# Kernel tuning notes

Hardware: AMD Instinct MI355X
Metric: run time of the kernel (lower is better)

## Reference

```python
import jax, jax.numpy as jnp
import numpy as np

BUCKETS = 256
B, CIN, H, W = 16, 64, 128, 128
COUT, K = 64, 3


def setup_inputs() -> dict:
    key = jax.random.key(0)
    k1, k2, k3, k4, k5 = jax.random.split(key, 5)
    x = jax.random.normal(k1, (B, CIN, H, W), dtype=jnp.float32)
    x_hash = jax.random.normal(k2, (B, CIN, H, W), dtype=jnp.float32)
    conv_weight = jax.random.normal(k3, (COUT, CIN, K, K), dtype=jnp.float32)
    hash_value = jnp.sort(jax.random.normal(k4, (BUCKETS,), dtype=jnp.float32))
    bias = jax.random.normal(k5, (COUT,), dtype=jnp.float32) * 0.1
    return {"x": x, "x_hash": x_hash, "conv_weight": conv_weight,
            "hash_value": hash_value, "bias": bias}


def _conv(x, w, b):
    # stride 1, padding 1 -> same spatial size (matches nn.Conv2d(padding=1))
    y = jax.lax.conv_general_dilated(
        x, w, window_strides=(1, 1), padding=[(1, 1), (1, 1)],
        dimension_numbers=("NCHW", "OIHW", "NCHW"))
    return y + b[None, :, None, None]


def _hash_weights(conv_weight, hash_value):
    # Uniform bucketization of weights into BUCKETS bins over [min, max],
    # then gather of the learned per-bucket hash value.
    w_min = jnp.min(conv_weight)
    w_max = jnp.max(conv_weight)
    width = (w_max - w_min) / BUCKETS
    idx = jnp.floor((conv_weight - w_min) / width).astype(jnp.int32)
    # w == max floors to BUCKETS; torch code assigns it the last bucket.
    idx = jnp.clip(idx, 0, BUCKETS - 1)
    return jnp.take(hash_value, idx)


def reference(x, x_hash, conv_weight, hash_value, bias):
    hash_weight = _hash_weights(conv_weight, hash_value)
    out = _conv(x, conv_weight, bias)
    hash_out = _conv(x, hash_weight, bias)
    out_hash = _conv(x_hash, hash_weight, bias)
    return (out, hash_out, out_hash)
```

## Files before the change

kernel.cpp:

```cpp
#include <hip/hip_runtime.h>
#include <stdint.h>

typedef short short8_t __attribute__((ext_vector_type(8)));
typedef float f32x4    __attribute__((ext_vector_type(4)));

__device__ __forceinline__ unsigned short f2bf(float f) {
  unsigned int u = __float_as_uint(f);
  u += 0x7FFFu + ((u >> 16) & 1u);
  return (unsigned short)(u >> 16);
}

__device__ __forceinline__ void glld16(const void* src, char* lds) {
  __builtin_amdgcn_global_load_lds(
      (const __attribute__((address_space(1))) void*)src,
      (__attribute__((address_space(3))) void*)lds, 16, 0, 0);
}

__device__ __forceinline__ short8_t lds_rd(const char* smem, int a) {
  int aa = a ^ (((a >> 7) & 7) << 4);
  return *(const short8_t*)(smem + aa);
}

__global__ __launch_bounds__(256) void minmax_kernel(const float* __restrict__ w,
                                                     float* __restrict__ mm) {
  int tid = threadIdx.x;
  float mn = 1e30f, mx = -1e30f;
  const float4* w4 = (const float4*)w;
  for (int i = tid; i < 9216; i += 256) {
    float4 v = w4[i];
    mn = fminf(mn, fminf(fminf(v.x, v.y), fminf(v.z, v.w)));
    mx = fmaxf(mx, fmaxf(fmaxf(v.x, v.y), fmaxf(v.z, v.w)));
  }
  for (int off = 32; off; off >>= 1) {
    mn = fminf(mn, __shfl_down(mn, off));
    mx = fmaxf(mx, __shfl_down(mx, off));
  }
  __shared__ float smn[4], smx[4];
  if ((tid & 63) == 0) { smn[tid >> 6] = mn; smx[tid >> 6] = mx; }
  __syncthreads();
  if (tid == 0) {
    mn = fminf(fminf(smn[0], smn[1]), fminf(smn[2], smn[3]));
    mx = fmaxf(fmaxf(smx[0], smx[1]), fmaxf(smx[2], smx[3]));
    mm[0] = mn; mm[1] = mx;
  }
}

__global__ __launch_bounds__(256) void hashprep_kernel(const float* __restrict__ w,
                                                       const float* __restrict__ hv,
                                                       const float* __restrict__ mm,
                                                       unsigned short* __restrict__ w0,
                                                       unsigned short* __restrict__ w1) {
  int t = blockIdx.x * 256 + threadIdx.x;
  if (t >= 36864) return;
  float mn = mm[0], mx = mm[1];
  float width = (mx - mn) / 256.0f;
  float wv = w[t];
  int idx = (int)floorf((wv - mn) / width);
  idx = min(max(idx, 0), 255);
  float hw = hv[idx];
  int co  = t / 576;
  int rem = t - co * 576;
  int ci  = rem / 9;
  int tap = rem - ci * 9;
  int dst = (tap * 64 + co) * 64 + ci;
  w0[dst] = f2bf(wv);
  w1[dst] = f2bf(hw);
}

__global__ __launch_bounds__(256) void xprep_kernel(const float* __restrict__ x,
                                                    unsigned short* __restrict__ xbf) {
  int t = blockIdx.x * 256 + threadIdx.x;
  int c8 = t & 7;
  int w  = (t >> 3) % 130;
  int bh = (t >> 3) / 130;
  short8_t v;
  #pragma unroll
  for (int j = 0; j < 8; ++j) v[j] = 0;
  if (w != 0 && w != 129) {
    const float* p = x + (((size_t)(bh >> 7) * 64 + c8 * 8) * 128 + (bh & 127)) * 128 + (w - 1);
    #pragma unroll
    for (int j = 0; j < 8; ++j) v[j] = (short)f2bf(p[(size_t)j * 16384]);
  }
  *(short8_t*)(xbf + (size_t)t * 8) = v;
}

#define XROW 16640
#define WSB  99840

template<int NSETS>
__global__ __launch_bounds__(512, 2) void conv_kernel(
    const unsigned short* __restrict__ xbf,
    const char* __restrict__ zeropage,
    const unsigned short* __restrict__ wg0,
    const unsigned short* __restrict__ wg1,
    const float* __restrict__ bias,
    float* __restrict__ out0,
    float* __restrict__ out1) {

  extern __shared__ char smem[];
  const int BUFSTRIDE = NSETS * 8192;

  int tid = threadIdx.x, lane = tid & 63, wv = tid >> 6;
  int m = lane & 15, g = (lane >> 4) & 3;
  int rr = wv >> 1, wseg = (wv & 1) << 6;

  int bx = blockIdx.x;
  int b = bx >> 5, h0 = (bx & 31) << 2;

  const char* xb = (const char*)xbf + (size_t)b * (130 * 128 * 128);
  for (int batch = wv; batch < 98; batch += 8) {
    int q = batch * 64 + lane;
    if (q < 6240) {
      int r    = q / 1040;
      int o_in = (q - r * 1040) << 4;
      int swz  = o_in ^ (((q >> 3) & 7) << 4);
      int hin  = h0 + r - 1;
      const char* src = ((unsigned)hin < 128u) ? (xb + (size_t)hin * XROW + swz)
                                               : (zeropage + swz);
      glld16(src, smem + batch * 1024);
    }
  }

  auto stage_w = [&](int t, int buf) {
    for (int batch = wv; batch < NSETS * 8; batch += 8) {
      int q    = batch * 64 + lane;
      int s    = q >> 9;
      int o_in = (q & 511) << 4;
      int key  = (4 + (q >> 3)) & 7;
      int swz  = o_in ^ (key << 4);
      const char* src = (const char*)(s ? wg1 : wg0) + t * 8192 + swz;
      glld16(src, smem + WSB + buf * BUFSTRIDE + batch * 1024);
    }
  };

  f32x4 acc[NSETS][4][4];
  #pragma unroll
  for (int s = 0; s < NSETS; ++s)
    #pragma unroll
    for (int i = 0; i < 4; ++i)
      #pragma unroll
      for (int j = 0; j < 4; ++j) acc[s][i][j] = (f32x4){0.f, 0.f, 0.f, 0.f};

  int arow[4], bcol[4];
  #pragma unroll
  for (int i = 0; i < 4; ++i) {
    arow[i] = ((i * 16 + m) << 7) + (g << 4);
    bcol[i] = ((wseg + i * 16 + m) << 7) + (g << 4);
  }

  stage_w(0, 0);
  __syncthreads();

  #pragma unroll
  for (int t = 0; t < 9; ++t) {
    if (t < 8) stage_w(t + 1, (t + 1) & 1);
    int kh = t / 3, kw = t - kh * 3;
    int xtap  = (rr + kh) * XROW + (kw << 7);
    int wbase = WSB + (t & 1) * BUFSTRIDE;
    #pragma unroll
    for (int ks = 0; ks < 2; ++ks) {
      int ko = ks << 6;
      short8_t bf[4];
      #pragma unroll
      for (int nf = 0; nf < 4; ++nf) bf[nf] = lds_rd(smem, xtap + bcol[nf] + ko);
      #pragma unroll
      for (int mt = 0; mt < 4; ++mt) {
        short8_t a0 = lds_rd(smem, wbase + arow[mt] + ko);
        #pragma unroll
        for (int nf = 0; nf < 4; ++nf)
          acc[0][mt][nf] = __builtin_amdgcn_mfma_f32_16x16x32_bf16(a0, bf[nf], acc[0][mt][nf], 0, 0, 0);
        if (NSETS == 2) {
          short8_t a1 = lds_rd(smem, wbase + 8192 + arow[mt] + ko);
          #pragma unroll
          for (int nf = 0; nf < 4; ++nf)
            acc[1][mt][nf] = __builtin_amdgcn_mfma_f32_16x16x32_bf16(a1, bf[nf], acc[1][mt][nf], 0, 0, 0);
        }
      }
    }
    __syncthreads();
  }

  size_t ob = (size_t)b * 64 * 16384 + (size_t)(h0 + rr) * 128 + wseg;
  #pragma unroll
  for (int s = 0; s < NSETS; ++s) {
    float* op = s ? out1 : out0;
    #pragma unroll
    for (int mt = 0; mt < 4; ++mt)
      #pragma unroll
      for (int r4 = 0; r4 < 4; ++r4) {
        int co = mt * 16 + g * 4 + r4;
        float bv = bias[co];
        #pragma unroll
        for (int nf = 0; nf < 4; ++nf)
          op[ob + (size_t)co * 16384 + nf * 16 + m] = acc[s][mt][nf][r4] + bv;
      }
  }
}

extern "C" void kernel_launch(void* const* d_in, const int* in_sizes, int n_in,
                              void* d_out, int out_size, void* d_ws, size_t ws_size,
                              hipStream_t stream) {
  const float* x    = (const float*)d_in[0];
  const float* xh   = (const float*)d_in[1];
  const float* cw   = (const float*)d_in[2];
  const float* hv   = (const float*)d_in[3];
  const float* bias = (const float*)d_in[4];

  float* out      = (float*)d_out;
  float* hash_out = out + 16777216;
  float* out_hash = out + 33554432;

  char* ws = (char*)d_ws;
  float* mm            = (float*)ws;
  char* zeropage       = ws + 128;
  unsigned short* w0   = (unsigned short*)(ws + 32768);
  unsigned short* w1   = (unsigned short*)(ws + 32768 + 73728);
  unsigned short* xbf  = (unsigned short*)(ws + 180224);

  hipMemsetAsync(zeropage, 0, 16640, stream);
  minmax_kernel<<<1, 256, 0, stream>>>(cw, mm);
  hashprep_kernel<<<144, 256, 0, stream>>>(cw, hv, mm, w0, w1);

  (void)hipFuncSetAttribute((const void*)conv_kernel<2>,
                            hipFuncAttributeMaxDynamicSharedMemorySize, 99840 + 32768);
  (void)hipFuncSetAttribute((const void*)conv_kernel<1>,
                            hipFuncAttributeMaxDynamicSharedMemorySize, 99840 + 16384);

  xprep_kernel<<<8320, 256, 0, stream>>>(x, xbf);
  conv_kernel<2><<<512, 512, 99840 + 32768, stream>>>(xbf, zeropage, w0, w1, bias, out, hash_out);
  xprep_kernel<<<8320, 256, 0, stream>>>(xh, xbf);
  conv_kernel<1><<<512, 512, 99840 + 16384, stream>>>(xbf, zeropage, w1, w1, bias, out_hash, out_hash);
}
```

Measured before the change: 389.1 us.

## Hold conv weights in registers, shrink conv tiles, transpose input via LDS

Weights are repacked into MFMA fragment order so each wave loads its A operands straight from global memory into registers per tap. This removes the double-buffered LDS weight staging and the per-tap barriers. The conv block shrinks to 256 threads covering 4 rows by 64 columns, with static LDS and a remapped block order. The input conversion now reads coalesced float4 rows and transposes through shared memory. The trade-offs are higher VGPR pressure, redundant weight loads from global/L2 in every wave, and more halo overlap from narrower tiles.

```diff
diff --git a/kernel.cpp b/kernel.cpp
--- a/kernel.cpp
+++ b/kernel.cpp
@@ -2,6 +2,7 @@
 #include <stdint.h>
 
 typedef short short8_t __attribute__((ext_vector_type(8)));
+typedef unsigned short ushort2_t __attribute__((ext_vector_type(2)));
 typedef float f32x4    __attribute__((ext_vector_type(4)));
 
 __device__ __forceinline__ unsigned short f2bf(float f) {
@@ -55,132 +56,143 @@
   float mn = mm[0], mx = mm[1];
   float width = (mx - mn) / 256.0f;
   float wv = w[t];
-  int idx = (int)floorf((wv - mn) / width);
-  idx = min(max(idx, 0), 255);
+  int idx = min(max((int)floorf((wv - mn) / width), 0), 255);
   float hw = hv[idx];
   int co  = t / 576;
   int rem = t - co * 576;
   int ci  = rem / 9;
   int tap = rem - ci * 9;
-  int dst = (tap * 64 + co) * 64 + ci;
+  int mt = co >> 4, m = co & 15;
+  int ks = ci >> 5, g = (ci & 31) >> 3, e = ci & 7;
+  int dst = ((tap * 8 + mt * 2 + ks) * 64 + g * 16 + m) * 8 + e;
   w0[dst] = f2bf(wv);
   w1[dst] = f2bf(hw);
 }
 
 __global__ __launch_bounds__(256) void xprep_kernel(const float* __restrict__ x,
                                                     unsigned short* __restrict__ xbf) {
-  int t = blockIdx.x * 256 + threadIdx.x;
-  int c8 = t & 7;
-  int w  = (t >> 3) % 130;
-  int bh = (t >> 3) / 130;
-  short8_t v;
-  #pragma unroll
-  for (int j = 0; j < 8; ++j) v[j] = 0;
-  if (w != 0 && w != 129) {
-    const float* p = x + (((size_t)(bh >> 7) * 64 + c8 * 8) * 128 + (bh & 127)) * 128 + (w - 1);
-    #pragma unroll
-    for (int j = 0; j < 8; ++j) v[j] = (short)f2bf(p[(size_t)j * 16384]);
-  }
-  *(short8_t*)(xbf + (size_t)t * 8) = v;
-}
-
-#define XROW 16640
-#define WSB  99840
+  __shared__ unsigned short T[64 * 130];
+  int t  = threadIdx.x;
+  int bh = blockIdx.x;
+  int b = bh >> 7, h = bh & 127;
+  const f32x4* x4 = (const f32x4*)x;
+  size_t xrow = (((size_t)(b * 64) * 128 + h) << 5);
+  #pragma unroll
+  for (int k = 0; k < 8; ++k) {
+    int j = k * 256 + t;
+    int c = j >> 5, w4 = j & 31;
+    f32x4 v = x4[xrow + ((size_t)c << 12) + w4];
+    ushort2_t lo, hi;
+    lo[0] = f2bf(v[0]); lo[1] = f2bf(v[1]);
+    hi[0] = f2bf(v[2]); hi[1] = f2bf(v[3]);
+    *(ushort2_t*)&T[c * 130 + w4 * 4]     = lo;
+    *(ushort2_t*)&T[c * 130 + w4 * 4 + 2] = hi;
+  }
+  __syncthreads();
+  size_t rb = (size_t)bh * (130 * 64);
+  if (t < 16) {
+    short8_t z = {0, 0, 0, 0, 0, 0, 0, 0};
+    int col = (t < 8) ? 0 : 129, ch = t & 7;
+    *(short8_t*)(xbf + rb + col * 64 + ch * 8) = z;
+  }
+  #pragma unroll
+  for (int k = 0; k < 4; ++k) {
+    int q = k * 256 + t;
+    int w = q >> 3, o8 = (q & 7) * 8;
+    short8_t v;
+    #pragma unroll
+    for (int j = 0; j < 8; ++j) v[j] = (short)T[(o8 + j) * 130 + w];
+    *(short8_t*)(xbf + rb + (size_t)(w + 1) * 64 + o8) = v;
+  }
+}
+
+#define XR 8448
 
 template<int NSETS>
-__global__ __launch_bounds__(512, 2) void conv_kernel(
+__global__ __launch_bounds__(256, 2) void conv_kernel(
     const unsigned short* __restrict__ xbf,
     const char* __restrict__ zeropage,
-    const unsigned short* __restrict__ wg0,
-    const unsigned short* __restrict__ wg1,
+    const unsigned short* __restrict__ wf0,
+    const unsigned short* __restrict__ wf1,
     const float* __restrict__ bias,
     float* __restrict__ out0,
     float* __restrict__ out1) {
 
-  extern __shared__ char smem[];
-  const int BUFSTRIDE = NSETS * 8192;
+  __shared__ char smem[6 * XR];
 
   int tid = threadIdx.x, lane = tid & 63, wv = tid >> 6;
-  int m = lane & 15, g = (lane >> 4) & 3;
-  int rr = wv >> 1, wseg = (wv & 1) << 6;
-
-  int bx = blockIdx.x;
-  int b = bx >> 5, h0 = (bx & 31) << 2;
-
-  const char* xb = (const char*)xbf + (size_t)b * (130 * 128 * 128);
-  for (int batch = wv; batch < 98; batch += 8) {
+  int m = lane & 15, g = lane >> 4;
+
+  int bx0 = blockIdx.x;
+  int bx  = (bx0 & 7) * 128 + (bx0 >> 3);
+  int b = bx >> 6, rowblk = (bx >> 1) & 31, wblk = bx & 1;
+  int h0 = rowblk * 4, W0 = wblk * 64;
+
+  const unsigned short* wsrc[2] = {wf0, wf1};
+
+  short8_t aw[NSETS][8];
+  #pragma unroll
+  for (int s = 0; s < NSETS; ++s)
+    #pragma unroll
+    for (int i = 0; i < 8; ++i)
+      aw[s][i] = *(const short8_t*)(wsrc[s] + i * 512 + lane * 8);
+
+  const char* xb = (const char*)xbf + (size_t)b * (130 * 128 * 128) + (size_t)W0 * 128;
+  for (int batch = wv; batch < 50; batch += 4) {
     int q = batch * 64 + lane;
-    if (q < 6240) {
-      int r    = q / 1040;
-      int o_in = (q - r * 1040) << 4;
-      int swz  = o_in ^ (((q >> 3) & 7) << 4);
-      int hin  = h0 + r - 1;
-      const char* src = ((unsigned)hin < 128u) ? (xb + (size_t)hin * XROW + swz)
+    if (q < 3168) {
+      int r = q / 528;
+      int o = (q - r * 528) << 4;
+      int swz = o ^ (((q >> 3) & 7) << 4);
+      int hin = h0 + r - 1;
+      const char* src = ((unsigned)hin < 128u) ? (xb + (size_t)hin * 16640 + swz)
                                                : (zeropage + swz);
       glld16(src, smem + batch * 1024);
     }
   }
 
-  auto stage_w = [&](int t, int buf) {
-    for (int batch = wv; batch < NSETS * 8; batch += 8) {
-      int q    = batch * 64 + lane;
-      int s    = q >> 9;
-      int o_in = (q & 511) << 4;
-      int key  = (4 + (q >> 3)) & 7;
-      int swz  = o_in ^ (key << 4);
-      const char* src = (const char*)(s ? wg1 : wg0) + t * 8192 + swz;
-      glld16(src, smem + WSB + buf * BUFSTRIDE + batch * 1024);
+  f32x4 acc[NSETS][4][4];
+  #pragma unroll
+  for (int s = 0; s < NSETS; ++s)
+    #pragma unroll
+    for (int i = 0; i < 4; ++i)
+      #pragma unroll
+      for (int j = 0; j < 4; ++j) acc[s][i][j] = (f32x4){0.f, 0.f, 0.f, 0.f};
+
+  int bcol[4];
+  #pragma unroll
+  for (int nf = 0; nf < 4; ++nf) bcol[nf] = ((nf * 16 + m) << 7) + (g << 4);
+
+  __syncthreads();
+
+  #pragma unroll
+  for (int t = 0; t < 9; ++t) {
+    if (t) {
+      #pragma unroll
+      for (int s = 0; s < NSETS; ++s)
+        #pragma unroll
+        for (int i = 0; i < 8; ++i)
+          aw[s][i] = *(const short8_t*)(wsrc[s] + t * 4096 + i * 512 + lane * 8);
     }
-  };
-
-  f32x4 acc[NSETS][4][4];
-  #pragma unroll
-  for (int s = 0; s < NSETS; ++s)
-    #pragma unroll
-    for (int i = 0; i < 4; ++i)
-      #pragma unroll
-      for (int j = 0; j < 4; ++j) acc[s][i][j] = (f32x4){0.f, 0.f, 0.f, 0.f};
-
-  int arow[4], bcol[4];
-  #pragma unroll
-  for (int i = 0; i < 4; ++i) {
-    arow[i] = ((i * 16 + m) << 7) + (g << 4);
-    bcol[i] = ((wseg + i * 16 + m) << 7) + (g << 4);
-  }
-
-  stage_w(0, 0);
-  __syncthreads();
-
-  #pragma unroll
-  for (int t = 0; t < 9; ++t) {
-    if (t < 8) stage_w(t + 1, (t + 1) & 1);
     int kh = t / 3, kw = t - kh * 3;
-    int xtap  = (rr + kh) * XROW + (kw << 7);
-    int wbase = WSB + (t & 1) * BUFSTRIDE;
+    int xtap = (wv + kh) * XR + (kw << 7);
     #pragma unroll
     for (int ks = 0; ks < 2; ++ks) {
-      int ko = ks << 6;
       short8_t bf[4];
       #pragma unroll
-      for (int nf = 0; nf < 4; ++nf) bf[nf] = lds_rd(smem, xtap + bcol[nf] + ko);
-      #pragma unroll
-      for (int mt = 0; mt < 4; ++mt) {
-        short8_t a0 = lds_rd(smem, wbase + arow[mt] + ko);
+      for (int nf = 0; nf < 4; ++nf) bf[nf] = lds_rd(smem, xtap + bcol[nf] + (ks << 6));
+      #pragma unroll
+      for (int s = 0; s < NSETS; ++s)
         #pragma unroll
-        for (int nf = 0; nf < 4; ++nf)
-          acc[0][mt][nf] = __builtin_amdgcn_mfma_f32_16x16x32_bf16(a0, bf[nf], acc[0][mt][nf], 0, 0, 0);
-        if (NSETS == 2) {
-          short8_t a1 = lds_rd(smem, wbase + 8192 + arow[mt] + ko);
+        for (int mt = 0; mt < 4; ++mt)
           #pragma unroll
           for (int nf = 0; nf < 4; ++nf)
-            acc[1][mt][nf] = __builtin_amdgcn_mfma_f32_16x16x32_bf16(a1, bf[nf], acc[1][mt][nf], 0, 0, 0);
-        }
-      }
+            acc[s][mt][nf] = __builtin_amdgcn_mfma_f32_16x16x32_bf16(
+                aw[s][mt * 2 + ks], bf[nf], acc[s][mt][nf], 0, 0, 0);
     }
-    __syncthreads();
-  }
-
-  size_t ob = (size_t)b * 64 * 16384 + (size_t)(h0 + rr) * 128 + wseg;
+  }
+
+  size_t ob = (size_t)b * 64 * 16384 + (size_t)(h0 + wv) * 128 + W0;
   #pragma unroll
   for (int s = 0; s < NSETS; ++s) {
     float* op = s ? out1 : out0;
@@ -213,21 +225,16 @@
   char* ws = (char*)d_ws;
   float* mm            = (float*)ws;
   char* zeropage       = ws + 128;
-  unsigned short* w0   = (unsigned short*)(ws + 32768);
-  unsigned short* w1   = (unsigned short*)(ws + 32768 + 73728);
+  unsigned short* w0F  = (unsigned short*)(ws + 32768);
+  unsigned short* w1F  = (unsigned short*)(ws + 32768 + 73728);
   unsigned short* xbf  = (unsigned short*)(ws + 180224);
 
   hipMemsetAsync(zeropage, 0, 16640, stream);
   minmax_kernel<<<1, 256, 0, stream>>>(cw, mm);
-  hashprep_kernel<<<144, 256, 0, stream>>>(cw, hv, mm, w0, w1);
-
-  (void)hipFuncSetAttribute((const void*)conv_kernel<2>,
-                            hipFuncAttributeMaxDynamicSharedMemorySize, 99840 + 32768);
-  (void)hipFuncSetAttribute((const void*)conv_kernel<1>,
-                            hipFuncAttributeMaxDynamicSharedMemorySize, 99840 + 16384);
-
-  xprep_kernel<<<8320, 256, 0, stream>>>(x, xbf);
-  conv_kernel<2><<<512, 512, 99840 + 32768, stream>>>(xbf, zeropage, w0, w1, bias, out, hash_out);
-  xprep_kernel<<<8320, 256, 0, stream>>>(xh, xbf);
-  conv_kernel<1><<<512, 512, 99840 + 16384, stream>>>(xbf, zeropage, w1, w1, bias, out_hash, out_hash);
-}
+  hashprep_kernel<<<144, 256, 0, stream>>>(cw, hv, mm, w0F, w1F);
+
+  xprep_kernel<<<2048, 256, 0, stream>>>(x, xbf);
+  conv_kernel<2><<<1024, 256, 0, stream>>>(xbf, zeropage, w0F, w1F, bias, out, hash_out);
+  xprep_kernel<<<2048, 256, 0, stream>>>(xh, xbf);
+  conv_kernel<1><<<1024, 256, 0, stream>>>(xbf, zeropage, w1F, w1F, bias, out_hash, out_hash);
+}
```

New measurement: 392.0 us. Within noise of the previous version (+0.7%).
